# Performance work log

Hardware: AMD Instinct MI355X
Metric: run time of the kernel (lower is better)

Reference implementation:

```python
import jax, jax.numpy as jnp
import numpy as np

B, S, D, H, DH, E, DFF = 8, 512, 768, 12, 64, 8, 3072
EPS = 1e-12
SCALE = D ** -0.5  # note: original scales by hidden_size**-0.5, not head_dim


def _ln(x, g, b):
    m = x.mean(-1, keepdims=True)
    v = ((x - m) ** 2).mean(-1, keepdims=True)
    return (x - m) * jax.lax.rsqrt(v + EPS) * g + b


def _expert(x, mask, Wqkv_e, Wd_e, bd_e, g1, be1, W1_e, b1_e, W2_e, b2_e, g2, be2):
    b, s, d = x.shape
    # fused per-head QKV: (B,S,D) x (H,3*DH,D) -> (B,H,S,3*DH)
    qkv = jnp.einsum('bnd,hkd->bhnk', x, Wqkv_e)
    q, k, v = jnp.split(qkv, 3, axis=-1)  # each (B,H,S,DH)
    scores = jnp.einsum('bhid,bhjd->bhij', q, k) * SCALE
    scores = jnp.where(mask[:, None, None, :] == 0, -jnp.inf, scores)
    attn = jax.nn.softmax(scores, axis=-1)
    ctx = jnp.einsum('bhij,bhjd->bhid', attn, v)
    ctx = ctx.transpose(0, 2, 1, 3).reshape(b, s, d)  # concat heads
    att = ctx @ Wd_e.T + bd_e              # attention.dense output (pre-residual)
    feat = att.mean(axis=1)                # (B,D) routing feature (mean over seq)
    h = _ln(att + x, g1, be1)              # post-norm attention block
    ffn = jax.nn.gelu(h @ W1_e.T + b1_e, approximate=False) @ W2_e.T + b2_e
    out = _ln(h + ffn, g2, be2)            # post-norm FFN block (dropout = eval/identity)
    return out, feat


def setup_inputs() -> dict:
    key = jax.random.key(0)
    ks = jax.random.split(key, 8)
    s = 0.02
    return {
        'hidden_states': jax.random.normal(ks[0], (B, S, D), jnp.float32),
        'attention_mask': jnp.ones((B, S), jnp.int32),
        'Wqkv': jax.random.normal(ks[1], (E, H, 3 * DH, D), jnp.float32) * s,
        'Wd': jax.random.normal(ks[2], (E, D, D), jnp.float32) * s,
        'bd': jnp.zeros((E, D), jnp.float32),
        'ln1_g': jnp.ones((E, D), jnp.float32),
        'ln1_b': jnp.zeros((E, D), jnp.float32),
        'W1': jax.random.normal(ks[3], (E, DFF, D), jnp.float32) * s,
        'b1': jnp.zeros((E, DFF), jnp.float32),
        'W2': jax.random.normal(ks[4], (E, D, DFF), jnp.float32) * s,
        'b2': jnp.zeros((E, D), jnp.float32),
        'ln2_g': jnp.ones((E, D), jnp.float32),
        'ln2_b': jnp.zeros((E, D), jnp.float32),
        'centers': jax.random.normal(ks[5], (E, D), jnp.float32) * 0.1,
    }


def reference(hidden_states, attention_mask, Wqkv, Wd, bd, ln1_g, ln1_b,
              W1, b1, W2, b2, ln2_g, ln2_b, centers):
    outs, feats = [], []
    for e in range(centers.shape[0]):  # small fixed set of experts
        o, f = _expert(hidden_states, attention_mask, Wqkv[e], Wd[e], bd[e],
                       ln1_g[e], ln1_b[e], W1[e], b1[e], W2[e], b2[e],
                       ln2_g[e], ln2_b[e])
        outs.append(o)
        feats.append(f)
    outs = jnp.stack(outs)    # (E,B,S,D)
    feats = jnp.stack(feats)  # (E,B,D)
    dists = jnp.linalg.norm(feats - centers[:, None, :], axis=-1)  # (E,B) torch.dist
    sel = jnp.argmin(dists, axis=0)  # (B,) hard routing
    return outs[sel, jnp.arange(outs.shape[1])]  # (B,S,D)
```

## Files before the change

### kernel.cpp

```cpp
#include <hip/hip_runtime.h>
#include <hip/hip_fp16.h>
#include <math.h>
#include <stdint.h>

#define Bb 8
#define Ss 512
#define Dd 768
#define Hh 12
#define Ee 8
#define DFF 3072
#define MROWS 4096
#define QKVN 2304

static __device__ const float SCALE_ = 0.036084391824351615f;
static __device__ const float SC2_   = 0.05206262648008056f;

typedef short bf8_t __attribute__((ext_vector_type(8)));
typedef _Float16 f16x4_t __attribute__((ext_vector_type(4)));
typedef float f32x4_t __attribute__((ext_vector_type(4)));

__device__ __forceinline__ float bf2f(unsigned short u){
  union { unsigned int i; float f; } x; x.i = ((unsigned int)u)<<16; return x.f;
}
__device__ __forceinline__ unsigned short f2bf(float f){
  union { float f; unsigned int i; } x; x.f = f;
  unsigned int u = x.i;
  return (unsigned short)((u + 0x7fffu + ((u>>16)&1u)) >> 16);
}

__device__ __forceinline__ void gl_lds16(const void* g, void* l){
  __builtin_amdgcn_global_load_lds(
      (const __attribute__((address_space(1))) unsigned int*)(g),
      (__attribute__((address_space(3))) unsigned int*)(uintptr_t)(l),
      16, 0, 0);
}

__global__ void cast_kernel(const float* __restrict__ in, unsigned short* __restrict__ out, int n){
  int i = (blockIdx.x*256 + threadIdx.x)*4;
  if (i >= n) return;
  const float4 v = *(const float4*)(in + i);
  ushort4 o; o.x=f2bf(v.x); o.y=f2bf(v.y); o.z=f2bf(v.z); o.w=f2bf(v.w);
  *(ushort4*)(out + i) = o;
}

#define VMW6 asm volatile("s_waitcnt vmcnt(6)" ::: "memory")
#define VMW0 asm volatile("s_waitcnt vmcnt(0)" ::: "memory")
#define NOOP ((void)0)

#define STG_A(SL,H,KT) { char* d_ = smem + (SL)*32768 + (H)*16384 + w*1024;          \
    gl_lds16(aSrc[0] + (size_t)(H)*hK + (size_t)(KT)*64, d_);                        \
    gl_lds16(aSrc[1] + (size_t)(H)*hK + (size_t)(KT)*64, d_ + 8192); }
#define STG_B(SL,H,KT) { char* d_ = smem + 65536 + (SL)*32768 + (H)*16384 + w*1024;  \
    gl_lds16(bSrc[0] + (size_t)(H)*hK + (size_t)(KT)*64, d_);                        \
    gl_lds16(bSrc[1] + (size_t)(H)*hK + (size_t)(KT)*64, d_ + 8192); }

#define PHASE(SL, QM, QN, DO_A, STAGE, WAITC)                                        \
  {                                                                                  \
    STAGE;                                                                           \
    WAITC;                                                                           \
    __builtin_amdgcn_s_barrier();                                                    \
    asm volatile("" ::: "memory");                                                   \
    if (DO_A) {                                                                      \
      _Pragma("unroll") for (int i_=0;i_<4;i_++)                                     \
        _Pragma("unroll") for (int k_=0;k_<2;k_++)                                   \
          afr[i_][k_] = *(const bf8_t*)(smem + (SL)*32768 + (QM)*16384 + aoff[i_][k_]); \
    }                                                                                \
    _Pragma("unroll") for (int j_=0;j_<2;j_++)                                       \
      _Pragma("unroll") for (int k_=0;k_<2;k_++)                                     \
        bfr[j_][k_] = *(const bf8_t*)(smem + (SL)*32768 + (QN)*16384 + boff[j_][k_]); \
    asm volatile("s_waitcnt lgkmcnt(0)" ::: "memory");                               \
    __builtin_amdgcn_sched_barrier(0);                                               \
    __builtin_amdgcn_s_setprio(1);                                                   \
    _Pragma("unroll") for (int k_=0;k_<2;k_++)                                       \
      _Pragma("unroll") for (int i_=0;i_<4;i_++)                                     \
        _Pragma("unroll") for (int j_=0;j_<2;j_++)                                   \
          acc[QM][QN][i_][j_] = __builtin_amdgcn_mfma_f32_16x16x32_bf16(             \
              afr[i_][k_], bfr[j_][k_], acc[QM][QN][i_][j_], 0,0,0);                 \
    __builtin_amdgcn_s_setprio(0);                                                   \
    __builtin_amdgcn_s_barrier();                                                    \
  }

__global__ __launch_bounds__(512, 2)
void gemm8p(const unsigned short* __restrict__ A,
            const unsigned short* __restrict__ B,
            unsigned short* __restrict__ C,
            int K, int N, long bStrideZ, long cStrideZ, int swz)
{
  extern __shared__ char smem[];
  const int t = threadIdx.x;
  const int w = t>>6, l = t&63, q4 = l>>4, mr = l&15;
  const int wm = w>>2, wn = w&3;

  int ct, rt, zz;
  if (swz == 1) {
    const int id = (blockIdx.z*gridDim.y + blockIdx.y)*gridDim.x + blockIdx.x;
    const int xcd = id & 7, slot = id >> 3;
    zz = xcd; ct = slot % gridDim.x; rt = slot / gridDim.x;
  } else { ct = blockIdx.x; rt = blockIdx.y; zz = blockIdx.z; }

  const unsigned short* Ap = A + (size_t)rt*256*K;
  const unsigned short* Bp = B + (size_t)zz*bStrideZ + (size_t)ct*256*K;

  const unsigned short* aSrc[2];
  const unsigned short* bSrc[2];
  #pragma unroll
  for (int c=0;c<2;c++){
    const int o  = c*8192 + t*16;
    const int lb = o ^ (((o>>7)&7)<<4);
    const int row = lb>>7, kcol = (lb&127)>>1;
    aSrc[c] = Ap + (size_t)row*K + kcol;
    bSrc[c] = Bp + (size_t)row*K + kcol;
  }
  const size_t hK = (size_t)128*K;

  int aoff[4][2], boff[2][2];
  #pragma unroll
  for (int i=0;i<4;i++)
    #pragma unroll
    for (int kk=0;kk<2;kk++){
      const int row = wm*64 + i*16 + mr;
      int b_ = row*128 + kk*64 + q4*16;
      b_ ^= (row&7)<<4;
      aoff[i][kk] = b_;
    }
  #pragma unroll
  for (int j=0;j<2;j++)
    #pragma unroll
    for (int kk=0;kk<2;kk++){
      const int row = wn*32 + j*16 + mr;
      int b_ = row*128 + kk*64 + q4*16;
      b_ ^= (row&7)<<4;
      boff[j][kk] = 65536 + b_;
    }

  f32x4_t acc[2][2][4][2];
  #pragma unroll
  for (int a0=0;a0<2;a0++)
    #pragma unroll
    for (int a1=0;a1<2;a1++)
      #pragma unroll
      for (int a2=0;a2<4;a2++)
        #pragma unroll
        for (int a3=0;a3<2;a3++) acc[a0][a1][a2][a3] = (f32x4_t){0.f,0.f,0.f,0.f};

  bf8_t afr[4][2], bfr[2][2];

  STG_A(0,0,0); STG_A(0,1,0); STG_B(0,0,0); STG_B(0,1,0);
  STG_A(1,0,1); STG_B(1,1,1);

  const int NITER = K >> 7;
  for (int it = 0; it < NITER-1; ++it){
    const int t1 = 2*it+1, t2 = 2*it+2, t3 = 2*it+3;
    PHASE(0,0,0, 1, STG_A(1,1,t1), VMW6);
    PHASE(0,0,1, 0, STG_B(1,0,t1), NOOP);
    PHASE(0,1,1, 1, STG_A(0,0,t2), NOOP);
    PHASE(0,1,0, 0, STG_B(0,1,t2), NOOP);
    PHASE(1,0,0, 1, STG_A(0,1,t2), VMW6);
    PHASE(1,0,1, 0, STG_B(0,0,t2), NOOP);
    PHASE(1,1,1, 1, STG_A(1,0,t3), NOOP);
    PHASE(1,1,0, 0, STG_B(1,1,t3), NOOP);
  }
  {
    const int t1 = 2*NITER-1;
    PHASE(0,0,0, 1, STG_A(1,1,t1), VMW6);
    PHASE(0,0,1, 0, STG_B(1,0,t1), NOOP);
    PHASE(0,1,1, 1, NOOP, NOOP);
    PHASE(0,1,0, 0, NOOP, NOOP);
    PHASE(1,0,0, 1, NOOP, VMW0);
    PHASE(1,0,1, 0, NOOP, NOOP);
    PHASE(1,1,1, 1, NOOP, NOOP);
    PHASE(1,1,0, 0, NOOP, NOOP);
  }

  unsigned short* Cp = C + (size_t)zz*cStrideZ;
  #pragma unroll
  for (int qm=0;qm<2;qm++)
    #pragma unroll
    for (int qn=0;qn<2;qn++)
      #pragma unroll
      for (int i=0;i<4;i++)
        #pragma unroll
        for (int j=0;j<2;j++){
          const long mb = (long)rt*256 + qm*128 + wm*64 + i*16 + q4*4;
          const long n  = (long)ct*256 + qn*128 + wn*32 + j*16 + mr;
          #pragma unroll
          for (int r=0;r<4;r++)
            Cp[(mb+r)*N + n] = f2bf(acc[qm][qn][i][j][r]);
        }
}

template<int MODE>
__global__ __launch_bounds__(256)
void gemm_bt(const unsigned short* __restrict__ A,
             const unsigned short* __restrict__ Bbf,
             const float* __restrict__ Bf32,
             const float* __restrict__ bias,
             void* __restrict__ Cout,
             int K, int N,
             long bStrideZ, long cStrideZ,
             const int* __restrict__ sel,
             long selAStride, long selBStride, int selBiasStride,
             int swz)
{
  constexpr int BP = (MODE >= 2) ? 40 : 32;
  __shared__ unsigned short As[128*32];
  __shared__ unsigned short Bs[128*BP];

  int rt, ct, zz;
  if (swz == 1) {
    const int id = (blockIdx.z*gridDim.y + blockIdx.y)*gridDim.x + blockIdx.x;
    const int xcd = id & 7, slot = id >> 3;
    zz = xcd; ct = slot % gridDim.x; rt = slot / gridDim.x;
  } else if (swz == 2) {
    const int id = blockIdx.y*gridDim.x + blockIdx.x;
    const int xcd = id & 7, slot = id >> 3;
    rt = xcd*4 + (slot & 3); ct = slot >> 2; zz = 0;
  } else {
    rt = blockIdx.y; ct = blockIdx.x; zz = blockIdx.z;
  }

  const int t = threadIdx.x;
  const int w = t>>6, l = t&63, q4 = l>>4, mr = l&15;
  const int wm = (w&1)*64, wn = (w>>1)*64;
  const int sr = t>>2, cv = t&3;

  const unsigned short* Ap = A;
  const unsigned short* Bp = Bbf;
  const float* Bf_ = Bf32;
  const float* biasp = bias;
  if (MODE == 0) {
    Bp += (size_t)zz * bStrideZ;
  } else {
    const int ex = sel[rt>>2];
    if (MODE == 1) { Ap += (size_t)ex * selAStride; Bp += (size_t)ex * selBStride; }
    else           { Bf_ += (size_t)ex * selBStride; }
    biasp += (long)ex * selBiasStride;
  }

  f32x4_t acc[4][4];
  #pragma unroll
  for (int i=0;i<4;i++)
    #pragma unroll
    for (int j=0;j<4;j++) acc[i][j] = (f32x4_t){0.f,0.f,0.f,0.f};

  const unsigned short* gA = Ap + (size_t)(rt*128 + w*16 + (l>>2))*K + (l&3)*8;
  unsigned short* lA = As + w*512;
  const unsigned short* gB = nullptr;
  unsigned short* lB = Bs + w*512;
  if (MODE < 2) gB = Bp + (size_t)(ct*128 + w*16 + (l>>2))*K + (l&3)*8;

  for (int k0 = 0; k0 < K; k0 += 32) {
    uint4 b0, b1;
    if (MODE >= 2) {
      const float* Br0 = Bf_ + (long)(ct*128 + sr)*K + cv*8 + k0;
      const float* Br1 = Br0 + (long)64*K;
      float4 f0a = *(const float4*)Br0;  float4 f0b = *(const float4*)(Br0+4);
      float4 f1a = *(const float4*)Br1;  float4 f1b = *(const float4*)(Br1+4);
      union { unsigned short s[8]; uint4 v; } p0, p1;
      p0.s[0]=f2bf(f0a.x); p0.s[1]=f2bf(f0a.y); p0.s[2]=f2bf(f0a.z); p0.s[3]=f2bf(f0a.w);
      p0.s[4]=f2bf(f0b.x); p0.s[5]=f2bf(f0b.y); p0.s[6]=f2bf(f0b.z); p0.s[7]=f2bf(f0b.w);
      p1.s[0]=f2bf(f1a.x); p1.s[1]=f2bf(f1a.y); p1.s[2]=f2bf(f1a.z); p1.s[3]=f2bf(f1a.w);
      p1.s[4]=f2bf(f1b.x); p1.s[5]=f2bf(f1b.y); p1.s[6]=f2bf(f1b.z); p1.s[7]=f2bf(f1b.w);
      b0 = p0.v; b1 = p1.v;
    }
    __syncthreads();
    gl_lds16(gA + k0,                lA);
    gl_lds16(gA + (size_t)64*K + k0, lA + 2048);
    if (MODE < 2) {
      gl_lds16(gB + k0,                lB);
      gl_lds16(gB + (size_t)64*K + k0, lB + 2048);
    } else {
      *(uint4*)&Bs[sr*40 + cv*8]      = b0;
      *(uint4*)&Bs[(sr+64)*40 + cv*8] = b1;
    }
    __syncthreads();
    bf8_t af[4], bfv[4];
    #pragma unroll
    for (int i=0;i<4;i++) af[i]  = *(const bf8_t*)&As[(wm+i*16+mr)*32 + q4*8];
    #pragma unroll
    for (int j=0;j<4;j++) bfv[j] = *(const bf8_t*)&Bs[(wn+j*16+mr)*BP + q4*8];
    #pragma unroll
    for (int i=0;i<4;i++)
      #pragma unroll
      for (int j=0;j<4;j++)
        acc[i][j] = __builtin_amdgcn_mfma_f32_16x16x32_bf16(af[i], bfv[j], acc[i][j], 0,0,0);
  }

  const long Cld = N;
  unsigned short* Cb16 = (unsigned short*)Cout + (size_t)zz * cStrideZ;
  float* Cf32 = (float*)Cout;
  #pragma unroll
  for (int j=0;j<4;j++){
    const int n = ct*128 + wn + j*16 + mr;
    const float bv = (MODE==0) ? 0.f : biasp[n];
    #pragma unroll
    for (int i=0;i<4;i++){
      const long mbase = (long)rt*128 + wm + i*16 + q4*4;
      #pragma unroll
      for (int r=0;r<4;r++){
        const float v = acc[i][j][r] + bv;
        const long m = mbase + r;
        if (MODE==0 || MODE==1) {
          Cb16[m*Cld + n] = f2bf(v);
        } else if (MODE==2) {
          const float g = 0.5f*v*(1.0f + erff(v*0.70710678118654752f));
          Cb16[m*Cld + n] = f2bf(g);
        } else {
          Cf32[m*Cld + n] = v;
        }
      }
    }
  }
}

__global__ __launch_bounds__(256)
void attn_kernel(const unsigned short* __restrict__ qkv,
                 const int* __restrict__ mask,
                 unsigned short* __restrict__ ctx,
                 long qkvStrideZ, long ctxStrideZ, int swz)
{
  int qb, h, zz;
  if (swz) {
    const int id = (blockIdx.z*gridDim.y + blockIdx.y)*gridDim.x + blockIdx.x;
    const int xcd = id & 7, slot = id >> 3;
    const int sz = slot / 96, sxy = slot % 96;
    qb = sxy & 7; h = sxy >> 3; zz = xcd*8 + sz;
  } else { qb = blockIdx.x; h = blockIdx.y; zz = blockIdx.z; }
  const int b = zz & 7, e = zz >> 3;
  qkv += (size_t)e * qkvStrideZ;
  ctx += (size_t)e * ctxStrideZ;

  const int t = threadIdx.x, w = t>>6, l = t&63, q4 = l>>4, mr = l&15;
  __shared__ float maskf[512];
  __shared__ unsigned short Ks[16*72];
  __shared__ unsigned short Vs[64*20];

  for (int i=t;i<512;i+=256) maskf[i] = mask[b*512 + i] ? 1.0f : 0.0f;

  const int srow = b*512 + qb*64 + w*16;
  const unsigned short* qp = qkv + (long)(srow+mr)*QKVN + h*192;
  const bf8_t qf0 = *(const bf8_t*)(qp + q4*8);
  const bf8_t qf1 = *(const bf8_t*)(qp + 32 + q4*8);

  f32x4_t cacc[4];
  #pragma unroll
  for (int d=0; d<4; d++) cacc[d] = (f32x4_t){0.f,0.f,0.f,0.f};
  float lsum = 0.f;

  const int el   = t*4;
  const int skey = el>>6;
  const int sd   = el&63;
  const unsigned short* kbase = qkv + (long)(b*512 + skey)*QKVN + h*192 + 64 + sd;
  const long kstep = (long)16*QKVN;

  uint2 kv = *(const uint2*)(kbase);
  uint2 vv = *(const uint2*)(kbase + 64);

  for (int kt=0; kt<32; kt++){
    __syncthreads();
    *(uint2*)&Ks[skey*72 + sd] = kv;
    {
      const unsigned short* pv = (const unsigned short*)&vv;
      #pragma unroll
      for (int jj=0;jj<4;jj++){
        const __half hv = __float2half(bf2f(pv[jj]));
        Vs[(sd+jj)*20 + skey] = __half_as_ushort(hv);
      }
    }
    if (kt < 31){
      kv = *(const uint2*)(kbase + (long)(kt+1)*kstep);
      vv = *(const uint2*)(kbase + (long)(kt+1)*kstep + 64);
    }
    __syncthreads();

    const bf8_t kf0 = *(const bf8_t*)&Ks[mr*72 + q4*8];
    const bf8_t kf1 = *(const bf8_t*)&Ks[mr*72 + 32 + q4*8];
    f32x4_t st = __builtin_amdgcn_mfma_f32_16x16x32_bf16(kf0, qf0, (f32x4_t){0.f,0.f,0.f,0.f}, 0,0,0);
    st = __builtin_amdgcn_mfma_f32_16x16x32_bf16(kf1, qf1, st, 0,0,0);

    const f32x4_t mv = *(const f32x4_t*)&maskf[kt*16 + q4*4];
    f16x4_t pf;
    #pragma unroll
    for (int r=0;r<4;r++){
      const float p = __builtin_exp2f(st[r]*SC2_) * mv[r];
      lsum += p;
      pf[r] = (_Float16)p;
    }
    #pragma unroll
    for (int dblk=0; dblk<4; dblk++){
      const f16x4_t vf = *(const f16x4_t*)&Vs[(dblk*16+mr)*20 + q4*4];
      cacc[dblk] = __builtin_amdgcn_mfma_f32_16x16x16f16(pf, vf, cacc[dblk], 0,0,0);
    }
  }

  lsum += __shfl_xor(lsum, 16);
  lsum += __shfl_xor(lsum, 32);
  #pragma unroll
  for (int r=0;r<4;r++){
    const int m2 = q4*4 + r;
    const float lr = __shfl(lsum, m2);
    const float inv = 1.0f/lr;
    const long orow = (long)(b*512 + qb*64 + w*16 + m2)*Dd + h*64;
    #pragma unroll
    for (int dblk=0; dblk<4; dblk++){
      ctx[orow + dblk*16 + mr] = f2bf(cacc[dblk][r]*inv);
    }
  }
}

__global__ void ctxmean_kernel(const unsigned short* __restrict__ ctx, float* __restrict__ out){
  const int d = blockIdx.x*256 + threadIdx.x;
  const int b = blockIdx.y, e = blockIdx.z;
  const unsigned short* p = ctx + ((size_t)e*MROWS + b*512)*Dd + d;
  float s = 0.f;
  for (int i=0;i<512;i++) s += bf2f(p[(size_t)i*Dd]);
  out[((size_t)e*Bb + b)*Dd + d] = s * (1.0f/512.0f);
}

__global__ __launch_bounds__(256)
void featgemm_kernel(const float* __restrict__ ctxmean, const unsigned short* __restrict__ Wdb,
                     const float* __restrict__ bd, float* __restrict__ feat){
  __shared__ float xs[Dd];
  const int b = blockIdx.x, e = blockIdx.y;
  const int t = threadIdx.x;
  for (int i=t;i<Dd;i+=256) xs[i] = ctxmean[((size_t)e*Bb+b)*Dd + i];
  __syncthreads();
  #pragma unroll
  for (int c0=0;c0<3;c0++){
    const int col = c0*256 + t;
    const unsigned short* wr = Wdb + ((size_t)e*Dd + col)*Dd;
    float s = 0.f;
    for (int k=0;k<Dd;k+=8){
      bf8_t wv = *(const bf8_t*)(wr + k);
      const unsigned short* wp = (const unsigned short*)&wv;
      #pragma unroll
      for (int j=0;j<8;j++) s += bf2f(wp[j]) * xs[k+j];
    }
    feat[((size_t)e*Bb+b)*Dd + col] = s + bd[(size_t)e*Dd + col];
  }
}

__global__ void routing_kernel(const float* __restrict__ feat, const float* __restrict__ centers,
                               int* __restrict__ sel)
{
  __shared__ float d2s[64];
  const int t = threadIdx.x;
  if (t < 64){
    const int e = t>>3, b = t&7;
    const float* f = feat + (long)(e*Bb + b)*Dd;
    const float* c = centers + (long)e*Dd;
    float s = 0.f;
    for (int d=0; d<Dd; d++){
      const float df = f[d] - c[d];
      s += df*df;
    }
    d2s[t] = s;
  }
  __syncthreads();
  if (t < 8){
    float best = 3.4e38f; int bi = 0;
    for (int e=0;e<8;e++){ const float v = d2s[e*8+t]; if (v < best){ best=v; bi=e; } }
    sel[t] = bi;
  }
}

__global__ __launch_bounds__(256)
void hprep_kernel(const unsigned short* __restrict__ attsel, const float* __restrict__ x,
                  const float* __restrict__ g, const float* __restrict__ be,
                  const int* __restrict__ sel, unsigned short* __restrict__ hbuf)
{
  const int w = threadIdx.x>>6, l = threadIdx.x&63;
  const int row = blockIdx.x*4 + w;
  const int b = row>>9;
  const int e = sel[b];
  const unsigned short* ap = attsel + (long)row*Dd;
  const float* xp = x + (long)row*Dd;
  float v[12]; float s = 0.f;
  #pragma unroll
  for (int i=0;i<12;i++){ const int d = i*64 + l; v[i] = bf2f(ap[d]) + xp[d]; s += v[i]; }
  #pragma unroll
  for (int o=32;o>0;o>>=1) s += __shfl_xor(s, o);
  const float mean = s * (1.0f/768.0f);
  float vs = 0.f;
  #pragma unroll
  for (int i=0;i<12;i++){ const float dd = v[i]-mean; vs += dd*dd; }
  #pragma unroll
  for (int o=32;o>0;o>>=1) vs += __shfl_xor(vs, o);
  const float rs = rsqrtf(vs*(1.0f/768.0f) + 1e-12f);
  #pragma unroll
  for (int i=0;i<12;i++){
    const int d = i*64 + l;
    hbuf[(long)row*Dd + d] = f2bf((v[i]-mean)*rs*g[(long)e*Dd+d] + be[(long)e*Dd+d]);
  }
}

__global__ __launch_bounds__(256)
void ln2_kernel(const unsigned short* __restrict__ hbuf, const float* __restrict__ tbuf,
                const float* __restrict__ g, const float* __restrict__ be,
                const int* __restrict__ sel, float* __restrict__ out)
{
  const int w = threadIdx.x>>6, l = threadIdx.x&63;
  const int row = blockIdx.x*4 + w;
  const int b = row>>9;
  const int e = sel[b];
  const unsigned short* hp = hbuf + (long)row*Dd;
  const float* tp = tbuf + (long)row*Dd;
  float v[12]; float s = 0.f;
  #pragma unroll
  for (int i=0;i<12;i++){ const int d = i*64 + l; v[i] = bf2f(hp[d]) + tp[d]; s += v[i]; }
  #pragma unroll
  for (int o=32;o>0;o>>=1) s += __shfl_xor(s, o);
  const float mean = s * (1.0f/768.0f);
  float vs = 0.f;
  #pragma unroll
  for (int i=0;i<12;i++){ const float dd = v[i]-mean; vs += dd*dd; }
  #pragma unroll
  for (int o=32;o>0;o>>=1) vs += __shfl_xor(vs, o);
  const float rs = rsqrtf(vs*(1.0f/768.0f) + 1e-12f);
  #pragma unroll
  for (int i=0;i<12;i++){
    const int d = i*64 + l;
    out[(long)row*Dd + d] = (v[i]-mean)*rs*g[(long)e*Dd+d] + be[(long)e*Dd+d];
  }
}

extern "C" void kernel_launch(void* const* d_in, const int* in_sizes, int n_in,
                              void* d_out, int out_size, void* d_ws, size_t ws_size,
                              hipStream_t stream)
{
  const float* x      = (const float*)d_in[0];
  const int*   mask   = (const int*)d_in[1];
  const float* Wqkv   = (const float*)d_in[2];
  const float* Wd     = (const float*)d_in[3];
  const float* bd     = (const float*)d_in[4];
  const float* ln1g   = (const float*)d_in[5];
  const float* ln1b   = (const float*)d_in[6];
  const float* W1     = (const float*)d_in[7];
  const float* b1     = (const float*)d_in[8];
  const float* W2     = (const float*)d_in[9];
  const float* b2     = (const float*)d_in[10];
  const float* ln2g   = (const float*)d_in[11];
  const float* ln2b   = (const float*)d_in[12];
  const float* centers= (const float*)d_in[13];

  hipFuncSetAttribute((const void*)gemm8p, hipFuncAttributeMaxDynamicSharedMemorySize, 131072);

  int zc;
  if      (ws_size >= 258347264ull) zc = 8;
  else if (ws_size >= 182849792ull) zc = 4;
  else if (ws_size >= 145101056ull) zc = 2;
  else                              zc = 1;

  char* p = (char*)d_ws;
  auto carve = [&](size_t bytes)->char*{ char* r = p; p += ((bytes + 255) & ~(size_t)255); return r; };

  unsigned short* xb      = (unsigned short*)carve((size_t)MROWS*Dd*2);
  unsigned short* Wqkvb   = (unsigned short*)carve((size_t)Ee*QKVN*Dd*2);
  unsigned short* Wdb     = (unsigned short*)carve((size_t)Ee*Dd*Dd*2);
  float*          ctxmean = (float*)carve((size_t)Ee*Bb*Dd*4);
  float*          feat    = (float*)carve((size_t)Ee*Bb*Dd*4);
  int*            sel     = (int*)carve(256);
  unsigned short* hbuf    = (unsigned short*)carve((size_t)MROWS*Dd*2);
  unsigned short* attsel  = (unsigned short*)carve((size_t)MROWS*Dd*2);
  unsigned short* qkvchk  = (unsigned short*)carve((size_t)zc*MROWS*QKVN*2);
  unsigned short* ctx_all = (unsigned short*)carve((size_t)Ee*MROWS*Dd*2);
  unsigned short* Gbuf = attsel;
  float*          tbuf = (float*)ctx_all;

  cast_kernel<<<(MROWS*Dd/4 + 255)/256, 256, 0, stream>>>(x, xb, MROWS*Dd);
  cast_kernel<<<(Ee*QKVN*Dd/4 + 255)/256, 256, 0, stream>>>(Wqkv, Wqkvb, Ee*QKVN*Dd);
  cast_kernel<<<(Ee*Dd*Dd/4 + 255)/256, 256, 0, stream>>>(Wd, Wdb, Ee*Dd*Dd);

  const int nchunk = Ee / zc;
  for (int c = 0; c < nchunk; c++){
    gemm8p<<<dim3(QKVN/256, MROWS/256, zc), 512, 131072, stream>>>(
        xb, Wqkvb + (size_t)c*zc*QKVN*Dd, qkvchk,
        Dd, QKVN, (long)QKVN*Dd, (long)MROWS*QKVN, (zc==8) ? 1 : 0);
    attn_kernel<<<dim3(8, Hh, Bb*zc), 256, 0, stream>>>(
        qkvchk, mask, ctx_all + (size_t)c*zc*MROWS*Dd,
        (long)MROWS*QKVN, (long)MROWS*Dd, (zc==8) ? 1 : 0);
    ctxmean_kernel<<<dim3(3, Bb, zc), 256, 0, stream>>>(
        ctx_all + (size_t)c*zc*MROWS*Dd, ctxmean + (size_t)c*zc*Bb*Dd);
  }

  featgemm_kernel<<<dim3(Bb, Ee), 256, 0, stream>>>(ctxmean, Wdb, bd, feat);
  routing_kernel<<<1, 64, 0, stream>>>(feat, centers, sel);

  gemm_bt<1><<<dim3(Dd/128, MROWS/128, 1), 256, 0, stream>>>(
      ctx_all, Wdb, nullptr, bd, attsel, Dd, Dd, 0, 0,
      sel, (long)MROWS*Dd, (long)Dd*Dd, Dd, 2);

  hprep_kernel<<<MROWS/4, 256, 0, stream>>>(attsel, x, ln1g, ln1b, sel, hbuf);
  gemm_bt<2><<<dim3(DFF/128, MROWS/128, 1), 256, 0, stream>>>(
      hbuf, nullptr, W1, b1, Gbuf, Dd, DFF, 0, 0,
      sel, 0, (long)DFF*Dd, DFF, 2);
  gemm_bt<3><<<dim3(Dd/128, MROWS/128, 1), 256, 0, stream>>>(
      Gbuf, nullptr, W2, b2, tbuf, DFF, Dd, 0, 0,
      sel, 0, (long)Dd*DFF, Dd, 2);
  ln2_kernel<<<MROWS/4, 256, 0, stream>>>(hbuf, tbuf, ln2g, ln2b, sel, (float*)d_out);
}
```

Before: 781.9 us.

## Double attention key tile, swizzle K in LDS, transpose-read V via ds_read_b64_tr_b16

The attention kernel now processes 32 keys per iteration instead of 16, which halves the loop trips and the number of barriers. K tiles are stored in LDS with an XOR swizzle instead of padding. V is written with 128-bit stores into a blocked layout and read back with the hardware transpose-load instruction, replacing the earlier scalar transposed stores. The change relies on inline asm for ds_read_b64_tr_b16 (a gfx950 instruction) and an explicit waitcnt and sched barrier, so it is tied to that hardware and harder to maintain.

```diff
diff --git a/kernel.cpp b/kernel.cpp
--- a/kernel.cpp
+++ b/kernel.cpp
@@ -332,8 +332,8 @@
 
   const int t = threadIdx.x, w = t>>6, l = t&63, q4 = l>>4, mr = l&15;
   __shared__ float maskf[512];
-  __shared__ unsigned short Ks[16*72];
-  __shared__ unsigned short Vs[64*20];
+  __shared__ unsigned short Ks[32*64];
+  __shared__ unsigned short Vt[2048];
 
   for (int i=t;i<512;i+=256) maskf[i] = mask[b*512 + i] ? 1.0f : 0.0f;
 
@@ -347,50 +347,90 @@
   for (int d=0; d<4; d++) cacc[d] = (f32x4_t){0.f,0.f,0.f,0.f};
   float lsum = 0.f;
 
-  const int el   = t*4;
-  const int skey = el>>6;
-  const int sd   = el&63;
-  const unsigned short* kbase = qkv + (long)(b*512 + skey)*QKVN + h*192 + 64 + sd;
-  const long kstep = (long)16*QKVN;
-
-  uint2 kv = *(const uint2*)(kbase);
-  uint2 vv = *(const uint2*)(kbase + 64);
-
-  for (int kt=0; kt<32; kt++){
+  const int skey = t>>3;
+  const int sd   = (t&7)*8;
+  const unsigned short* kgp = qkv + (long)(b*512 + skey)*QKVN + h*192 + 64 + sd;
+  const unsigned short* vgp = kgp + 64;
+  const long kstep = (long)32*QKVN;
+
+  unsigned short* ksw = &Ks[skey*64 + (sd ^ ((skey&7)<<3))];
+  unsigned short* vsw = &Vt[(skey>>4)*1024 + (sd>>4)*256 + ((skey>>2)&3)*64 + (skey&3)*16 + (sd&15)];
+
+  const int kx  = (mr&7)<<3;
+  const int k00i = mr*64      + ((q4*8)      ^ kx);
+  const int k01i = mr*64      + ((32 + q4*8) ^ kx);
+  const int k10i = (16+mr)*64 + ((q4*8)      ^ kx);
+  const int k11i = (16+mr)*64 + ((32 + q4*8) ^ kx);
+
+  const unsigned trb = (unsigned)(uintptr_t)(&Vt[0]) + (unsigned)(l*8);
+
+  uint4 kreg = *(const uint4*)kgp;
+  uint4 vreg = *(const uint4*)vgp;
+
+  for (int kt=0; kt<16; kt++){
     __syncthreads();
-    *(uint2*)&Ks[skey*72 + sd] = kv;
+    *(uint4*)ksw = kreg;
     {
-      const unsigned short* pv = (const unsigned short*)&vv;
+      const unsigned short* pv = (const unsigned short*)&vreg;
+      union { unsigned short s[8]; uint4 v; } hh;
       #pragma unroll
-      for (int jj=0;jj<4;jj++){
-        const __half hv = __float2half(bf2f(pv[jj]));
-        Vs[(sd+jj)*20 + skey] = __half_as_ushort(hv);
-      }
-    }
-    if (kt < 31){
-      kv = *(const uint2*)(kbase + (long)(kt+1)*kstep);
-      vv = *(const uint2*)(kbase + (long)(kt+1)*kstep + 64);
+      for (int j=0;j<8;j++) hh.s[j] = __half_as_ushort(__float2half(bf2f(pv[j])));
+      *(uint4*)vsw = hh.v;
+    }
+    if (kt < 15){
+      kreg = *(const uint4*)(kgp + (long)(kt+1)*kstep);
+      vreg = *(const uint4*)(vgp + (long)(kt+1)*kstep);
     }
     __syncthreads();
 
-    const bf8_t kf0 = *(const bf8_t*)&Ks[mr*72 + q4*8];
-    const bf8_t kf1 = *(const bf8_t*)&Ks[mr*72 + 32 + q4*8];
-    f32x4_t st = __builtin_amdgcn_mfma_f32_16x16x32_bf16(kf0, qf0, (f32x4_t){0.f,0.f,0.f,0.f}, 0,0,0);
-    st = __builtin_amdgcn_mfma_f32_16x16x32_bf16(kf1, qf1, st, 0,0,0);
-
-    const f32x4_t mv = *(const f32x4_t*)&maskf[kt*16 + q4*4];
-    f16x4_t pf;
+    const f32x4_t m0 = *(const f32x4_t*)&maskf[kt*32 + q4*4];
+    const f32x4_t m1 = *(const f32x4_t*)&maskf[kt*32 + 16 + q4*4];
+    const bf8_t k00 = *(const bf8_t*)&Ks[k00i];
+    const bf8_t k01 = *(const bf8_t*)&Ks[k01i];
+    const bf8_t k10 = *(const bf8_t*)&Ks[k10i];
+    const bf8_t k11 = *(const bf8_t*)&Ks[k11i];
+    f32x4_t st0 = (f32x4_t){0.f,0.f,0.f,0.f};
+    f32x4_t st1 = (f32x4_t){0.f,0.f,0.f,0.f};
+    st0 = __builtin_amdgcn_mfma_f32_16x16x32_bf16(k00, qf0, st0, 0,0,0);
+    st0 = __builtin_amdgcn_mfma_f32_16x16x32_bf16(k01, qf1, st0, 0,0,0);
+    st1 = __builtin_amdgcn_mfma_f32_16x16x32_bf16(k10, qf0, st1, 0,0,0);
+    st1 = __builtin_amdgcn_mfma_f32_16x16x32_bf16(k11, qf1, st1, 0,0,0);
+
+    f16x4_t vA0, vA1, vA2, vA3, vB0, vB1, vB2, vB3;
+    asm volatile("ds_read_b64_tr_b16 %0, %1 offset:0"    : "=v"(vA0) : "v"(trb));
+    asm volatile("ds_read_b64_tr_b16 %0, %1 offset:512"  : "=v"(vA1) : "v"(trb));
+    asm volatile("ds_read_b64_tr_b16 %0, %1 offset:1024" : "=v"(vA2) : "v"(trb));
+    asm volatile("ds_read_b64_tr_b16 %0, %1 offset:1536" : "=v"(vA3) : "v"(trb));
+    asm volatile("ds_read_b64_tr_b16 %0, %1 offset:2048" : "=v"(vB0) : "v"(trb));
+    asm volatile("ds_read_b64_tr_b16 %0, %1 offset:2560" : "=v"(vB1) : "v"(trb));
+    asm volatile("ds_read_b64_tr_b16 %0, %1 offset:3072" : "=v"(vB2) : "v"(trb));
+    asm volatile("ds_read_b64_tr_b16 %0, %1 offset:3584" : "=v"(vB3) : "v"(trb));
+
+    f16x4_t pf0, pf1;
     #pragma unroll
     for (int r=0;r<4;r++){
-      const float p = __builtin_exp2f(st[r]*SC2_) * mv[r];
+      const float p = __builtin_exp2f(st0[r]*SC2_) * m0[r];
       lsum += p;
-      pf[r] = (_Float16)p;
-    }
-    #pragma unroll
-    for (int dblk=0; dblk<4; dblk++){
-      const f16x4_t vf = *(const f16x4_t*)&Vs[(dblk*16+mr)*20 + q4*4];
-      cacc[dblk] = __builtin_amdgcn_mfma_f32_16x16x16f16(pf, vf, cacc[dblk], 0,0,0);
-    }
+      pf0[r] = (_Float16)p;
+    }
+    #pragma unroll
+    for (int r=0;r<4;r++){
+      const float p = __builtin_exp2f(st1[r]*SC2_) * m1[r];
+      lsum += p;
+      pf1[r] = (_Float16)p;
+    }
+
+    asm volatile("s_waitcnt lgkmcnt(0)" ::: "memory");
+    __builtin_amdgcn_sched_barrier(0);
+
+    cacc[0] = __builtin_amdgcn_mfma_f32_16x16x16f16(pf0, vA0, cacc[0], 0,0,0);
+    cacc[1] = __builtin_amdgcn_mfma_f32_16x16x16f16(pf0, vA1, cacc[1], 0,0,0);
+    cacc[2] = __builtin_amdgcn_mfma_f32_16x16x16f16(pf0, vA2, cacc[2], 0,0,0);
+    cacc[3] = __builtin_amdgcn_mfma_f32_16x16x16f16(pf0, vA3, cacc[3], 0,0,0);
+    cacc[0] = __builtin_amdgcn_mfma_f32_16x16x16f16(pf1, vB0, cacc[0], 0,0,0);
+    cacc[1] = __builtin_amdgcn_mfma_f32_16x16x16f16(pf1, vB1, cacc[1], 0,0,0);
+    cacc[2] = __builtin_amdgcn_mfma_f32_16x16x16f16(pf1, vB2, cacc[2], 0,0,0);
+    cacc[3] = __builtin_amdgcn_mfma_f32_16x16x16f16(pf1, vB3, cacc[3], 0,0,0);
   }
 
   lsum += __shfl_xor(lsum, 16);
```

Result: no change. 777.7 us (-0.5%).
